# Optimization experiments

Hardware: AMD Instinct MI355X
Metric: run time of the kernel (lower is better)

The kernel has to match this reference:

```python
import jax, jax.numpy as jnp
import numpy as np

N_HEAD = 8
LINEAR_DIM = 64
IN_PIXELS = 4096  # h*w = 64*64
D = N_HEAD * LINEAR_DIM  # 512
C = 128
LN_EPS = 1e-6
BN_EPS = 1e-5


def setup_inputs() -> dict:
    key = jax.random.key(0)
    ks = jax.random.split(key, 10)
    shp = (16, C, 64, 64)
    # Kaiming-uniform-ish small init for weights (torch Linear weight layout: [out, in])
    def lin(k, out_f, in_f):
        lim = 1.0 / np.sqrt(in_f)
        return jax.random.uniform(k, (out_f, in_f), jnp.float32, -lim, lim)
    return {
        "v": jax.random.normal(ks[0], shp, jnp.float32),
        "k": jax.random.normal(ks[1], shp, jnp.float32),
        "q": jax.random.normal(ks[2], shp, jnp.float32),
        "w_qs": lin(ks[3], D, IN_PIXELS),
        "w_ks": lin(ks[4], D, IN_PIXELS),
        "w_vs": lin(ks[5], D, IN_PIXELS),
        "w_fc": lin(ks[6], IN_PIXELS, D),
        "ln_gamma": jnp.ones((D,), jnp.float32),
        "ln_beta": jnp.zeros((D,), jnp.float32),
        "temperature": jnp.asarray(IN_PIXELS ** 0.5, jnp.float32),
        "bn_gamma": jnp.ones((C,), jnp.float32),
        "bn_beta": jnp.zeros((C,), jnp.float32),
    }


def _layer_norm(x, gamma, beta):
    # torch-faithful: unbiased std (ddof=1), divide by (std + eps)
    mean = jnp.mean(x, axis=-1, keepdims=True)
    var = jnp.var(x, axis=-1, keepdims=True, ddof=1)
    std = jnp.sqrt(var)
    return gamma * (x - mean) / (std + LN_EPS) + beta


def reference(v, k, q, w_qs, w_ks, w_vs, w_fc, ln_gamma, ln_beta, temperature, bn_gamma, bn_beta):
    b, c, h, w = q.shape
    P = h * w
    qf = q.reshape(b, c, P)
    kf = k.reshape(b, c, P)
    vf = v.reshape(b, c, P)
    residual = vf
    # QKV projections: [b,c,P] @ W^T -> [b,c,D] -> [b,nh,c,ld]
    def proj(x, W):
        y = jnp.einsum('bcp,dp->bcd', x, W)
        return y.reshape(b, c, N_HEAD, LINEAR_DIM).transpose(0, 2, 1, 3)
    Q = proj(qf, w_qs)
    K = proj(kf, w_ks)
    V = proj(vf, w_vs)
    # channel-wise attention: scores [b,nh,c,c]
    scores = jnp.einsum('bhcd,bhed->bhce', Q / temperature, K)
    attn = jax.nn.softmax(scores, axis=-1)
    O = jnp.einsum('bhce,bhed->bhcd', attn, V)
    O = O.transpose(0, 2, 1, 3).reshape(b, c, N_HEAD * LINEAR_DIM)
    # Swish -> LayerNorm -> fc -> residual
    O = O * jax.nn.sigmoid(O)
    O = _layer_norm(O, ln_gamma, ln_beta)
    O = jnp.einsum('bcd,pd->bcp', O, w_fc)
    out = (residual + O).reshape(b, c, h, w)
    # BatchNorm2d in training mode: batch stats over (b,h,w), biased variance
    mean = jnp.mean(out, axis=(0, 2, 3), keepdims=True)
    var = jnp.var(out, axis=(0, 2, 3), keepdims=True)
    out = (out - mean) / jnp.sqrt(var + BN_EPS)
    out = out * bn_gamma[None, :, None, None] + bn_beta[None, :, None, None]
    return out
```

## Files before the change

kernel.cpp:

```cpp
#include <hip/hip_runtime.h>
#include <hip/hip_bf16.h>
#include <stdint.h>

typedef __attribute__((ext_vector_type(8))) short bf16x8;
typedef __attribute__((ext_vector_type(4))) float f32x4;

#define AS1(p) ((const __attribute__((address_space(1))) uint32_t*)(p))
#define AS3(p) ((__attribute__((address_space(3))) uint32_t*)(p))

#define VM12   asm volatile("s_waitcnt vmcnt(12)")
#define VM0    asm volatile("s_waitcnt vmcnt(0)")
#define LG0    asm volatile("s_waitcnt lgkmcnt(0)")
#define SBAR   __builtin_amdgcn_s_barrier()
#define SCHED0 __builtin_amdgcn_sched_barrier(0)

__device__ __forceinline__ ushort f2bf(float f) {
  uint32_t u = __float_as_uint(f);
  uint32_t r = (u + 0x7fffu + ((u >> 16) & 1u)) >> 16;
  return (ushort)r;
}

__device__ __forceinline__ float bf2f(ushort u) {
  uint32_t v = ((uint32_t)u) << 16;
  return __uint_as_float(v);
}

__device__ __forceinline__ uint4 cvt8u(float4 a0, float4 a1) {
  uint4 r;
  asm("v_cvt_pk_bf16_f32 %0, %1, %2" : "=v"(r.x) : "v"(a0.x), "v"(a0.y));
  asm("v_cvt_pk_bf16_f32 %0, %1, %2" : "=v"(r.y) : "v"(a0.z), "v"(a0.w));
  asm("v_cvt_pk_bf16_f32 %0, %1, %2" : "=v"(r.z) : "v"(a1.x), "v"(a1.y));
  asm("v_cvt_pk_bf16_f32 %0, %1, %2" : "=v"(r.w) : "v"(a1.z), "v"(a1.w));
  return r;
}

__global__ __launch_bounds__(256) void pack4(
    const float* __restrict__ s0, const float* __restrict__ s1,
    const float* __restrict__ s2, const float* __restrict__ s3,
    ushort* __restrict__ o0, ushort* __restrict__ o1,
    ushort* __restrict__ o2, ushort* __restrict__ o3, int n)
{
  const float* s; ushort* o;
  switch (blockIdx.y) {
    case 0: s = s0; o = o0; break;
    case 1: s = s1; o = o1; break;
    case 2: s = s2; o = o2; break;
    default: s = s3; o = o3; break;
  }
  int stride = gridDim.x * 1024;
  for (int i = (blockIdx.x * 256 + threadIdx.x) * 4; i < n; i += stride) {
    float4 v = *(const float4*)(s + i);
    ushort4 u;
    u.x = f2bf(v.x); u.y = f2bf(v.y); u.z = f2bf(v.z); u.w = f2bf(v.w);
    *(ushort4*)(o + i) = u;
  }
}

__global__ __launch_bounds__(256, 3) void gemm_qkv(
    const float* __restrict__ aq, const float* __restrict__ ak, const float* __restrict__ av,
    const ushort* __restrict__ wq, const ushort* __restrict__ wk, const ushort* __restrict__ wv,
    ushort* __restrict__ part, int lgs)
{
  __shared__ __align__(16) ushort At[128 * 64];
  __shared__ __align__(16) ushort Bt[2][128 * 64];
  int per = gridDim.x >> 3;
  int bid = blockIdx.x;
  int swz = (bid & 7) * per + (bid >> 3);
  int y = swz & 3, x = (swz >> 2) & 15, zz = swz >> 6;
  int g = zz >> lgs, s = zz & ((1 << lgs) - 1);
  const float* A; const ushort* Bm;
  if (g == 0)      { A = aq; Bm = wq; }
  else if (g == 1) { A = ak; Bm = wk; }
  else             { A = av; Bm = wv; }
  ushort* Pd = part + ((size_t)zz) * 1048576;
  const int K = 4096;
  const int kchunk = K >> lgs;
  const int k0 = s * kchunk, kend = k0 + kchunk;
  int rowBase = x * 128;
  int colBase = y * 128;
  int tid = threadIdx.x, l = tid & 63, w = tid >> 6;
  int wr = w >> 1, wc = w & 1, fr = l & 15, fq = l >> 4;

  int arow = tid >> 3;
  int aslot = tid & 7;
  int aswz = aslot ^ (arow & 7);
  const float* Abase = A + (size_t)(rowBase + arow) * K + aslot * 8;
  char* At0 = (char*)At + arow * 128 + aswz * 16;

  f32x4 acc[4][4];
#pragma unroll
  for (int m = 0; m < 4; ++m)
#pragma unroll
    for (int n = 0; n < 4; ++n) acc[m][n] = (f32x4){0.f, 0.f, 0.f, 0.f};

  float4 a0, a1, a2, a3, a4, a5, a6, a7;

#define LOADA(ktn) do { \
    a0 = *(const float4*)(Abase + (size_t)0 * K + (ktn)); \
    a1 = *(const float4*)(Abase + (size_t)0 * K + (ktn) + 4); \
    a2 = *(const float4*)(Abase + (size_t)32 * K + (ktn)); \
    a3 = *(const float4*)(Abase + (size_t)32 * K + (ktn) + 4); \
    a4 = *(const float4*)(Abase + (size_t)64 * K + (ktn)); \
    a5 = *(const float4*)(Abase + (size_t)64 * K + (ktn) + 4); \
    a6 = *(const float4*)(Abase + (size_t)96 * K + (ktn)); \
    a7 = *(const float4*)(Abase + (size_t)96 * K + (ktn) + 4); \
  } while (0)

#define CVTWRITEA do { \
    *(uint4*)(At0 + 0 * 4096)  = cvt8u(a0, a1); \
    *(uint4*)(At0 + 1 * 4096)  = cvt8u(a2, a3); \
    *(uint4*)(At0 + 2 * 4096)  = cvt8u(a4, a5); \
    *(uint4*)(At0 + 3 * 4096)  = cvt8u(a6, a7); \
  } while (0)

#define STAGEB(bufIdx, ktn) do { \
    char* Bbuf_ = (char*)Bt[bufIdx]; \
    _Pragma("unroll") \
    for (int j = 0; j < 4; ++j) { \
      int c = ((w * 4 + j) << 6) + l; \
      int row = c >> 3, slot = c & 7; \
      int srccol = (slot ^ (row & 7)) * 8; \
      __builtin_amdgcn_global_load_lds(AS1(Bm + (size_t)(colBase + row) * K + (ktn) + srccol), \
                                       AS3(Bbuf_ + c * 16), 16, 0, 0); \
    } \
  } while (0)

#define MFMAPHASE(bufIdx) do { \
    const char* Bbuf_ = (const char*)Bt[bufIdx]; \
    _Pragma("unroll") \
    for (int kc = 0; kc < 2; ++kc) { \
      bf16x8 af[4], bv[4]; \
      _Pragma("unroll") \
      for (int m = 0; m < 4; ++m) { \
        int r = wr * 64 + m * 16 + fr; \
        int sl = (kc * 4 + fq) ^ (fr & 7); \
        af[m] = *(const bf16x8*)((const char*)At + r * 128 + sl * 16); \
      } \
      _Pragma("unroll") \
      for (int n = 0; n < 4; ++n) { \
        int r = wc * 64 + n * 16 + fr; \
        int sl = (kc * 4 + fq) ^ (fr & 7); \
        bv[n] = *(const bf16x8*)(Bbuf_ + r * 128 + sl * 16); \
      } \
      _Pragma("unroll") \
      for (int m = 0; m < 4; ++m) \
        _Pragma("unroll") \
        for (int n = 0; n < 4; ++n) \
          acc[m][n] = __builtin_amdgcn_mfma_f32_16x16x32_bf16(af[m], bv[n], acc[m][n], 0, 0, 0); \
    } \
  } while (0)

  LOADA(k0);
  STAGEB(0, k0);
  CVTWRITEA;
  LG0; SCHED0;

  int buf = 0;
#pragma unroll 1
  for (int kt = k0; kt < kend; kt += 64) {
    bool more = (kt + 64) < kend;
    if (more) {
      LOADA(kt + 64);
      STAGEB(buf ^ 1, kt + 64);
      VM12; SCHED0;
    } else {
      VM0; SCHED0;
    }
    SBAR; SCHED0;
    MFMAPHASE(buf);
    SBAR;
    if (more) {
      CVTWRITEA;
      LG0; SCHED0;
    }
    buf ^= 1;
  }

#undef LOADA
#undef CVTWRITEA
#undef STAGEB
#undef MFMAPHASE

#pragma unroll
  for (int m = 0; m < 4; ++m)
#pragma unroll
    for (int n = 0; n < 4; ++n)
#pragma unroll
      for (int r = 0; r < 4; ++r) {
        int row = rowBase + wr * 64 + m * 16 + fq * 4 + r;
        int col = colBase + wc * 64 + n * 16 + fr;
        Pd[(size_t)row * 512 + col] = f2bf(acc[m][n][r]);
      }
}

__global__ __launch_bounds__(256) void reduce_qkv(
    const ushort* __restrict__ part, ushort* __restrict__ Qp, ushort* __restrict__ Kp,
    ushort* __restrict__ Vp, int lgs)
{
  int g = blockIdx.y;
  ushort* dst = g == 0 ? Qp : (g == 1 ? Kp : Vp);
  const ushort* p = part + (((size_t)g) << lgs) * 1048576;
  int i = (blockIdx.x * 256 + threadIdx.x) * 8;
  int splits = 1 << lgs;
  float accv[8];
  {
    bf16x8 v = *(const bf16x8*)(p + i);
#pragma unroll
    for (int j = 0; j < 8; ++j) accv[j] = bf2f((ushort)v[j]);
  }
  for (int s = 1; s < splits; ++s) {
    bf16x8 v = *(const bf16x8*)(p + (size_t)s * 1048576 + i);
#pragma unroll
    for (int j = 0; j < 8; ++j) accv[j] += bf2f((ushort)v[j]);
  }
  ushort u[8];
#pragma unroll
  for (int j = 0; j < 8; ++j) u[j] = f2bf(accv[j]);
  *(uint4*)(dst + i) = *(uint4*)u;
}

__global__ __launch_bounds__(256) void attn(
    const ushort* __restrict__ Qp, const ushort* __restrict__ Kp, const ushort* __restrict__ Vp,
    float* __restrict__ Obuf, const float* __restrict__ temp)
{
  __shared__ __align__(16) ushort Qs[64 * 64];
  __shared__ __align__(16) ushort Ks[128 * 64];
  __shared__ __align__(16) ushort Vt[64 * 128];
  __shared__ __align__(16) float  Sl[64 * 128];
  __shared__ __align__(16) ushort Pl[64 * 128];
  __shared__ float rsum[64];
  int bh = blockIdx.y, b = bh >> 3, h = bh & 7;
  int c0 = blockIdx.x * 64;
  int tid = threadIdx.x, l = tid & 63, w = tid >> 6;
  int wr = w >> 1, wc = w & 1, fr = l & 15, fq = l >> 4;
  float invT = 1.0f / temp[0];
  const size_t rowQ = (size_t)(b * 128 + c0);

#pragma unroll
  for (int j = 0; j < 2; ++j) {
    int c = ((w * 2 + j) << 6) + l, row = c >> 3, cc = c & 7;
    __builtin_amdgcn_global_load_lds(AS1(Qp + (rowQ + row) * 512 + h * 64 + cc * 8),
                                     AS3((char*)Qs + (w * 2 + j) * 1024), 16, 0, 0);
  }
#pragma unroll
  for (int j = 0; j < 4; ++j) {
    int c = ((w * 4 + j) << 6) + l, row = c >> 3, cc = c & 7;
    __builtin_amdgcn_global_load_lds(AS1(Kp + (size_t)(b * 128 + row) * 512 + h * 64 + cc * 8),
                                     AS3((char*)Ks + (w * 4 + j) * 1024), 16, 0, 0);
  }
#pragma unroll
  for (int t = 0; t < 4; ++t) {
    int ch = tid + t * 256, e = ch >> 3, d0 = (ch & 7) * 8;
    bf16x8 vv = *(const bf16x8*)(Vp + (size_t)(b * 128 + e) * 512 + h * 64 + d0);
#pragma unroll
    for (int j = 0; j < 8; ++j) Vt[(d0 + j) * 128 + e] = (ushort)vv[j];
  }
  __syncthreads();

  f32x4 sa[2][4];
#pragma unroll
  for (int m = 0; m < 2; ++m)
#pragma unroll
    for (int n = 0; n < 4; ++n) sa[m][n] = (f32x4){0.f, 0.f, 0.f, 0.f};
#pragma unroll
  for (int kc = 0; kc < 2; ++kc) {
    bf16x8 aQ[2], bK[4];
#pragma unroll
    for (int m = 0; m < 2; ++m)
      aQ[m] = *(const bf16x8*)&Qs[(wr * 32 + m * 16 + fr) * 64 + kc * 32 + fq * 8];
#pragma unroll
    for (int n = 0; n < 4; ++n)
      bK[n] = *(const bf16x8*)&Ks[(wc * 64 + n * 16 + fr) * 64 + kc * 32 + fq * 8];
#pragma unroll
    for (int m = 0; m < 2; ++m)
#pragma unroll
      for (int n = 0; n < 4; ++n)
        sa[m][n] = __builtin_amdgcn_mfma_f32_16x16x32_bf16(aQ[m], bK[n], sa[m][n], 0, 0, 0);
  }
#pragma unroll
  for (int m = 0; m < 2; ++m)
#pragma unroll
    for (int n = 0; n < 4; ++n)
#pragma unroll
      for (int r = 0; r < 4; ++r)
        Sl[(wr * 32 + m * 16 + fq * 4 + r) * 128 + wc * 64 + n * 16 + fr] = sa[m][n][r] * invT;
  __syncthreads();

  {
    int row = tid >> 2, qq = tid & 3;
    const float* srow = Sl + row * 128 + qq * 32;
    float4 va[8];
#pragma unroll
    for (int i = 0; i < 8; ++i) va[i] = *(const float4*)(srow + i * 4);
    float mx = -1e30f;
#pragma unroll
    for (int i = 0; i < 8; ++i)
      mx = fmaxf(mx, fmaxf(fmaxf(va[i].x, va[i].y), fmaxf(va[i].z, va[i].w)));
    mx = fmaxf(mx, __shfl_xor(mx, 1));
    mx = fmaxf(mx, __shfl_xor(mx, 2));
    float ssum = 0.f;
    ushort* prow = Pl + row * 128 + qq * 32;
#pragma unroll
    for (int i = 0; i < 8; ++i) {
      float e0 = __expf(va[i].x - mx), e1 = __expf(va[i].y - mx);
      float e2 = __expf(va[i].z - mx), e3 = __expf(va[i].w - mx);
      ssum += (e0 + e1) + (e2 + e3);
      ushort4 u; u.x = f2bf(e0); u.y = f2bf(e1); u.z = f2bf(e2); u.w = f2bf(e3);
      *(ushort4*)(prow + i * 4) = u;
    }
    ssum += __shfl_xor(ssum, 1);
    ssum += __shfl_xor(ssum, 2);
    if (qq == 0) rsum[row] = ssum;
  }
  __syncthreads();

  f32x4 oa[2][2];
#pragma unroll
  for (int m = 0; m < 2; ++m)
#pragma unroll
    for (int n = 0; n < 2; ++n) oa[m][n] = (f32x4){0.f, 0.f, 0.f, 0.f};
#pragma unroll
  for (int kc = 0; kc < 4; ++kc) {
    bf16x8 aP[2], bV[2];
#pragma unroll
    for (int m = 0; m < 2; ++m)
      aP[m] = *(const bf16x8*)&Pl[(wr * 32 + m * 16 + fr) * 128 + kc * 32 + fq * 8];
#pragma unroll
    for (int n = 0; n < 2; ++n)
      bV[n] = *(const bf16x8*)&Vt[(wc * 32 + n * 16 + fr) * 128 + kc * 32 + fq * 8];
#pragma unroll
    for (int m = 0; m < 2; ++m)
#pragma unroll
      for (int n = 0; n < 2; ++n)
        oa[m][n] = __builtin_amdgcn_mfma_f32_16x16x32_bf16(aP[m], bV[n], oa[m][n], 0, 0, 0);
  }
#pragma unroll
  for (int m = 0; m < 2; ++m)
#pragma unroll
    for (int n = 0; n < 2; ++n)
#pragma unroll
      for (int r = 0; r < 4; ++r) {
        int row = wr * 32 + m * 16 + fq * 4 + r, col = wc * 32 + n * 16 + fr;
        Obuf[(rowQ + row) * 512 + h * 64 + col] = oa[m][n][r] / rsum[row];
      }
}

__global__ __launch_bounds__(256) void swish_ln(
    const float* __restrict__ O, ushort* __restrict__ X,
    const float* __restrict__ gamma, const float* __restrict__ beta)
{
  int row = blockIdx.x * 4 + (threadIdx.x >> 6);
  int lane = threadIdx.x & 63;
  const float* x = O + (size_t)row * 512 + lane * 8;
  float4 va = *(const float4*)(x);
  float4 vb = *(const float4*)(x + 4);
  float y[8] = {va.x, va.y, va.z, va.w, vb.x, vb.y, vb.z, vb.w};
  float s = 0.f, sq = 0.f;
#pragma unroll
  for (int i = 0; i < 8; ++i) {
    y[i] = y[i] / (1.f + __expf(-y[i]));
    s += y[i]; sq += y[i] * y[i];
  }
#pragma unroll
  for (int o = 1; o < 64; o <<= 1) { s += __shfl_xor(s, o); sq += __shfl_xor(sq, o); }
  float mean = s * (1.f / 512.f);
  float var = (sq - s * mean) * (1.f / 511.f);
  float inv = 1.f / (sqrtf(var) + 1e-6f);
  const float4 g0 = *(const float4*)(gamma + lane * 8);
  const float4 g1 = *(const float4*)(gamma + lane * 8 + 4);
  const float4 b0 = *(const float4*)(beta + lane * 8);
  const float4 b1 = *(const float4*)(beta + lane * 8 + 4);
  float gg[8] = {g0.x, g0.y, g0.z, g0.w, g1.x, g1.y, g1.z, g1.w};
  float bb[8] = {b0.x, b0.y, b0.z, b0.w, b1.x, b1.y, b1.z, b1.w};
  ushort u[8];
#pragma unroll
  for (int i = 0; i < 8; ++i) u[i] = f2bf(gg[i] * (y[i] - mean) * inv + bb[i]);
  *(uint4*)(X + (size_t)row * 512 + lane * 8) = *(uint4*)u;
}

__global__ __launch_bounds__(256) void gemm_fc(
    const ushort* __restrict__ A, const ushort* __restrict__ Bm,
    const float* __restrict__ resid, ushort* __restrict__ valb,
    float* __restrict__ bn_sum, float* __restrict__ bn_sq)
{
  __shared__ __align__(16) ushort At[128 * 64];
  __shared__ __align__(16) ushort Bt[128 * 64];
  __shared__ float csum[128], csq[128];
  const int K = 512;
  int rowBase = blockIdx.x * 128;
  int colBase = blockIdx.y * 128;
  int tid = threadIdx.x, l = tid & 63, w = tid >> 6;
  int wr = w >> 1, wc = w & 1, fr = l & 15, fq = l >> 4;
  if (tid < 128) { csum[tid] = 0.f; csq[tid] = 0.f; }
  f32x4 acc[4][4];
#pragma unroll
  for (int m = 0; m < 4; ++m)
#pragma unroll
    for (int n = 0; n < 4; ++n) acc[m][n] = (f32x4){0.f, 0.f, 0.f, 0.f};

  for (int kt = 0; kt < K; kt += 64) {
#pragma unroll
    for (int j = 0; j < 4; ++j) {
      int c = ((w * 4 + j) << 6) + l;
      int row = c >> 3, cc = c & 7;
      __builtin_amdgcn_global_load_lds(AS1(A + (size_t)(rowBase + row) * K + kt + cc * 8),
                                       AS3((char*)At + (w * 4 + j) * 1024), 16, 0, 0);
      __builtin_amdgcn_global_load_lds(AS1(Bm + (size_t)(colBase + row) * K + kt + cc * 8),
                                       AS3((char*)Bt + (w * 4 + j) * 1024), 16, 0, 0);
    }
    __syncthreads();
#pragma unroll
    for (int kc = 0; kc < 2; ++kc) {
      bf16x8 af[4], bfv[4];
#pragma unroll
      for (int m = 0; m < 4; ++m)
        af[m] = *(const bf16x8*)&At[(wr * 64 + m * 16 + fr) * 64 + kc * 32 + fq * 8];
#pragma unroll
      for (int n = 0; n < 4; ++n)
        bfv[n] = *(const bf16x8*)&Bt[(wc * 64 + n * 16 + fr) * 64 + kc * 32 + fq * 8];
#pragma unroll
      for (int m = 0; m < 4; ++m)
#pragma unroll
        for (int n = 0; n < 4; ++n)
          acc[m][n] = __builtin_amdgcn_mfma_f32_16x16x32_bf16(af[m], bfv[n], acc[m][n], 0, 0, 0);
    }
    __syncthreads();
  }
#pragma unroll
  for (int m = 0; m < 4; ++m)
#pragma unroll
    for (int r = 0; r < 4; ++r) {
      float ps = 0.f, pq = 0.f;
#pragma unroll
      for (int n = 0; n < 4; ++n) {
        int row = rowBase + wr * 64 + m * 16 + fq * 4 + r;
        int col = colBase + wc * 64 + n * 16 + fr;
        size_t idx = (size_t)row * 4096 + col;
        float val = acc[m][n][r] + resid[idx];
        valb[idx] = f2bf(val);
        ps += val; pq += val * val;
      }
#pragma unroll
      for (int o = 1; o < 16; o <<= 1) { ps += __shfl_xor(ps, o); pq += __shfl_xor(pq, o); }
      if (fr == 0) {
        int ch = wr * 64 + m * 16 + fq * 4 + r;
        atomicAdd(&csum[ch], ps);
        atomicAdd(&csq[ch], pq);
      }
    }
  __syncthreads();
  if (tid < 128) {
    atomicAdd(&bn_sum[tid], csum[tid]);
    atomicAdd(&bn_sq[tid], csq[tid]);
  }
}

__global__ __launch_bounds__(256) void bn_norm(
    const ushort* __restrict__ valb, float* __restrict__ out,
    const float* __restrict__ bn_sum, const float* __restrict__ bn_sq,
    const float* __restrict__ gamma, const float* __restrict__ beta)
{
  __shared__ float sc[128], sh[128];
  const float inv_n = 1.f / 65536.f;
  int tid = threadIdx.x;
  if (tid < 128) {
    float mean = bn_sum[tid] * inv_n;
    float var = bn_sq[tid] * inv_n - mean * mean;
    float g = gamma[tid] * rsqrtf(var + 1e-5f);
    sc[tid] = g;
    sh[tid] = beta[tid] - mean * g;
  }
  __syncthreads();
  int stride = gridDim.x * blockDim.x;
  for (int v = blockIdx.x * blockDim.x + tid; v < 1048576; v += stride) {
    int elem = v * 8;
    int ch = (elem >> 12) & 127;
    float g = sc[ch], bta = sh[ch];
    bf16x8 x = *(const bf16x8*)(valb + elem);
    float4 o0, o1;
    o0.x = bf2f((ushort)x[0]) * g + bta;
    o0.y = bf2f((ushort)x[1]) * g + bta;
    o0.z = bf2f((ushort)x[2]) * g + bta;
    o0.w = bf2f((ushort)x[3]) * g + bta;
    o1.x = bf2f((ushort)x[4]) * g + bta;
    o1.y = bf2f((ushort)x[5]) * g + bta;
    o1.z = bf2f((ushort)x[6]) * g + bta;
    o1.w = bf2f((ushort)x[7]) * g + bta;
    *(float4*)(out + elem) = o0;
    *(float4*)(out + elem + 4) = o1;
  }
}

extern "C" void kernel_launch(void* const* d_in, const int* in_sizes, int n_in,
                              void* d_out, int out_size, void* d_ws, size_t ws_size,
                              hipStream_t stream)
{
  const float* v_in = (const float*)d_in[0];
  const float* k_in = (const float*)d_in[1];
  const float* q_in = (const float*)d_in[2];
  const float* w_qs = (const float*)d_in[3];
  const float* w_ks = (const float*)d_in[4];
  const float* w_vs = (const float*)d_in[5];
  const float* w_fc = (const float*)d_in[6];
  const float* ln_g = (const float*)d_in[7];
  const float* ln_b = (const float*)d_in[8];
  const float* temp = (const float*)d_in[9];
  const float* bn_g = (const float*)d_in[10];
  const float* bn_b = (const float*)d_in[11];
  float* out = (float*)d_out;

  char* ws = (char*)d_ws;
  size_t off = 0;
  auto alloc = [&](size_t bytes) { char* p = ws + off; off += bytes; return p; };
  ushort* wq  = (ushort*)alloc(512ull * 4096 * 2);
  ushort* wk  = (ushort*)alloc(512ull * 4096 * 2);
  ushort* wv  = (ushort*)alloc(512ull * 4096 * 2);
  ushort* wfc = (ushort*)alloc(512ull * 4096 * 2);
  ushort* Qp  = (ushort*)alloc(2048ull * 512 * 2);
  ushort* Kp  = (ushort*)alloc(2048ull * 512 * 2);
  ushort* Vp  = (ushort*)alloc(2048ull * 512 * 2);
  float*  Obuf= (float*)alloc(2048ull * 512 * 4);
  ushort* X16 = (ushort*)alloc(2048ull * 512 * 2);
  ushort* valb= (ushort*)alloc(2048ull * 4096 * 2);
  float*  bns = (float*)alloc(128 * 4);
  float*  bnq = (float*)alloc(128 * 4);

  int lgs = 2;
  while (lgs > 0 && off + (3ull << lgs) * 1048576 * 2 > ws_size) --lgs;
  ushort* part = (ushort*)alloc((3ull << lgs) * 1048576 * 2);

  hipMemsetAsync(bns, 0, 256 * 4, stream);

  pack4<<<dim3(512, 4), 256, 0, stream>>>(w_qs, w_ks, w_vs, w_fc, wq, wk, wv, wfc,
                                          512 * 4096);
  gemm_qkv<<<16 * 4 * (3 << lgs), 256, 0, stream>>>(q_in, k_in, v_in, wq, wk, wv, part, lgs);
  reduce_qkv<<<dim3(512, 3), 256, 0, stream>>>(part, Qp, Kp, Vp, lgs);
  attn<<<dim3(2, 128), 256, 0, stream>>>(Qp, Kp, Vp, Obuf, temp);
  swish_ln<<<512, 256, 0, stream>>>(Obuf, X16, ln_g, ln_b);
  gemm_fc<<<dim3(16, 32), 256, 0, stream>>>(X16, wfc, v_in, valb, bns, bnq);
  bn_norm<<<2048, 256, 0, stream>>>(valb, out, bns, bnq, bn_g, bn_b);
}
```

Measured before the change: 115.0 us.

## Fuse fc GEMM with BatchNorm via cooperative grid sync

Adds a cooperative kernel that computes the fc GEMM plus residual, accumulates per-channel batch statistics, waits on a grid-wide sync, then applies the BatchNorm normalization straight from the accumulators held in registers. This removes the bf16 intermediate write and re-read and the separate bn_norm launch. In exchange all 512 blocks must be co-resident (two per CU), which the launch-bounds hint requests, and the grid sync adds a global barrier. It also skips the bf16 rounding of the intermediate that the old path applied.

New measurement: 115.7 us. Within noise of the previous version (+0.6%).

```diff
diff --git a/kernel.cpp b/kernel.cpp
--- a/kernel.cpp
+++ b/kernel.cpp
@@ -1,6 +1,9 @@
 #include <hip/hip_runtime.h>
 #include <hip/hip_bf16.h>
+#include <hip/hip_cooperative_groups.h>
 #include <stdint.h>
+
+namespace cg = cooperative_groups;
 
 typedef __attribute__((ext_vector_type(8))) short bf16x8;
 typedef __attribute__((ext_vector_type(4))) float f32x4;
@@ -378,6 +381,111 @@
   *(uint4*)(X + (size_t)row * 512 + lane * 8) = *(uint4*)u;
 }
 
+__global__ __launch_bounds__(256, 2) void gemm_fc_bn(
+    const ushort* __restrict__ A, const ushort* __restrict__ Bm,
+    const float* __restrict__ resid, float* __restrict__ out,
+    float* __restrict__ bn_sum, float* __restrict__ bn_sq,
+    const float* __restrict__ gamma, const float* __restrict__ beta)
+{
+  __shared__ __align__(16) ushort At[128 * 64];
+  __shared__ __align__(16) ushort Bt[128 * 64];
+  __shared__ float csum[128], csq[128];
+  const int K = 512;
+  int bid = blockIdx.x;
+  int rowBase = (bid >> 5) * 128;
+  int colBase = (bid & 31) * 128;
+  int tid = threadIdx.x, l = tid & 63, w = tid >> 6;
+  int wr = w >> 1, wc = w & 1, fr = l & 15, fq = l >> 4;
+  if (tid < 128) { csum[tid] = 0.f; csq[tid] = 0.f; }
+  f32x4 acc[4][4];
+#pragma unroll
+  for (int m = 0; m < 4; ++m)
+#pragma unroll
+    for (int n = 0; n < 4; ++n) acc[m][n] = (f32x4){0.f, 0.f, 0.f, 0.f};
+
+  for (int kt = 0; kt < K; kt += 64) {
+#pragma unroll
+    for (int j = 0; j < 4; ++j) {
+      int c = ((w * 4 + j) << 6) + l;
+      int row = c >> 3, cc = c & 7;
+      __builtin_amdgcn_global_load_lds(AS1(A + (size_t)(rowBase + row) * K + kt + cc * 8),
+                                       AS3((char*)At + (w * 4 + j) * 1024), 16, 0, 0);
+      __builtin_amdgcn_global_load_lds(AS1(Bm + (size_t)(colBase + row) * K + kt + cc * 8),
+                                       AS3((char*)Bt + (w * 4 + j) * 1024), 16, 0, 0);
+    }
+    __syncthreads();
+#pragma unroll
+    for (int kc = 0; kc < 2; ++kc) {
+      bf16x8 af[4], bfv[4];
+#pragma unroll
+      for (int m = 0; m < 4; ++m)
+        af[m] = *(const bf16x8*)&At[(wr * 64 + m * 16 + fr) * 64 + kc * 32 + fq * 8];
+#pragma unroll
+      for (int n = 0; n < 4; ++n)
+        bfv[n] = *(const bf16x8*)&Bt[(wc * 64 + n * 16 + fr) * 64 + kc * 32 + fq * 8];
+#pragma unroll
+      for (int m = 0; m < 4; ++m)
+#pragma unroll
+        for (int n = 0; n < 4; ++n)
+          acc[m][n] = __builtin_amdgcn_mfma_f32_16x16x32_bf16(af[m], bfv[n], acc[m][n], 0, 0, 0);
+    }
+    __syncthreads();
+  }
+#pragma unroll
+  for (int m = 0; m < 4; ++m)
+#pragma unroll
+    for (int r = 0; r < 4; ++r) {
+      float ps = 0.f, pq = 0.f;
+#pragma unroll
+      for (int n = 0; n < 4; ++n) {
+        int row = rowBase + wr * 64 + m * 16 + fq * 4 + r;
+        int col = colBase + wc * 64 + n * 16 + fr;
+        size_t idx = (size_t)row * 4096 + col;
+        float val = acc[m][n][r] + resid[idx];
+        acc[m][n][r] = val;
+        ps += val; pq += val * val;
+      }
+#pragma unroll
+      for (int o = 1; o < 16; o <<= 1) { ps += __shfl_xor(ps, o); pq += __shfl_xor(pq, o); }
+      if (fr == 0) {
+        int ch = wr * 64 + m * 16 + fq * 4 + r;
+        atomicAdd(&csum[ch], ps);
+        atomicAdd(&csq[ch], pq);
+      }
+    }
+  __syncthreads();
+  if (tid < 128) {
+    atomicAdd(&bn_sum[tid], csum[tid]);
+    atomicAdd(&bn_sq[tid], csq[tid]);
+  }
+
+  cg::this_grid().sync();
+
+  if (tid < 128) {
+    const float inv_n = 1.f / 65536.f;
+    float mean = bn_sum[tid] * inv_n;
+    float var = bn_sq[tid] * inv_n - mean * mean;
+    float gch = gamma[tid] * rsqrtf(var + 1e-5f);
+    csum[tid] = gch;
+    csq[tid] = beta[tid] - mean * gch;
+  }
+  __syncthreads();
+
+#pragma unroll
+  for (int m = 0; m < 4; ++m)
+#pragma unroll
+    for (int r = 0; r < 4; ++r) {
+      int ch = wr * 64 + m * 16 + fq * 4 + r;
+      float gch = csum[ch], bch = csq[ch];
+      int row = rowBase + ch;
+#pragma unroll
+      for (int n = 0; n < 4; ++n) {
+        int col = colBase + wc * 64 + n * 16 + fr;
+        out[(size_t)row * 4096 + col] = acc[m][n][r] * gch + bch;
+      }
+    }
+}
+
 __global__ __launch_bounds__(256) void gemm_fc(
     const ushort* __restrict__ A, const ushort* __restrict__ Bm,
     const float* __restrict__ resid, ushort* __restrict__ valb,
@@ -537,6 +645,19 @@
   reduce_qkv<<<dim3(512, 3), 256, 0, stream>>>(part, Qp, Kp, Vp, lgs);
   attn<<<dim3(2, 128), 256, 0, stream>>>(Qp, Kp, Vp, Obuf, temp);
   swish_ln<<<512, 256, 0, stream>>>(Obuf, X16, ln_g, ln_b);
-  gemm_fc<<<dim3(16, 32), 256, 0, stream>>>(X16, wfc, v_in, valb, bns, bnq);
-  bn_norm<<<2048, 256, 0, stream>>>(valb, out, bns, bnq, bn_g, bn_b);
-}
+
+  int maxb = 0;
+  hipError_t oe = hipOccupancyMaxActiveBlocksPerMultiprocessor(
+      &maxb, (const void*)gemm_fc_bn, 256, 0);
+  if (oe == hipSuccess && maxb >= 2) {
+    const ushort* a_ = X16; const ushort* b_ = wfc; const float* r_ = v_in;
+    float* o_ = out; float* s_ = bns; float* q_ = bnq;
+    const float* g_ = bn_g; const float* t_ = bn_b;
+    void* kargs[] = {&a_, &b_, &r_, &o_, &s_, &q_, &g_, &t_};
+    hipLaunchCooperativeKernel((const void*)gemm_fc_bn, dim3(512), dim3(256),
+                               kargs, 0, stream);
+  } else {
+    gemm_fc<<<dim3(16, 32), 256, 0, stream>>>(X16, wfc, v_in, valb, bns, bnq);
+    bn_norm<<<2048, 256, 0, stream>>>(valb, out, bns, bnq, bn_g, bn_b);
+  }
+}
```
